# Optimization experiments

Measured on AMD Instinct MI355X. Metric: run time of the kernel, lower is better.

Reference implementation:

```python
import jax, jax.numpy as jnp
import numpy as np

N_NODES = 200000
D = 256
HID = 512
OUT = 2
NUM_GRAPHS = 512


def setup_inputs() -> dict:
    key = jax.random.key(0)
    ks = jax.random.split(key, 8)
    x = jax.random.normal(ks[0], (N_NODES, D), dtype=jnp.float32)
    batch = jnp.sort(jax.random.randint(ks[1], (N_NODES,), 0, NUM_GRAPHS, dtype=jnp.int32))
    # MLP params (Linear stores weight as [out, in] in torch; we use [in, out])
    W1 = jax.random.normal(ks[2], (D, HID), dtype=jnp.float32) / np.sqrt(D)
    b1 = jnp.zeros((HID,), dtype=jnp.float32)
    W2 = jax.random.normal(ks[3], (HID, HID), dtype=jnp.float32) / np.sqrt(HID)
    b2 = jnp.zeros((HID,), dtype=jnp.float32)
    W3 = jax.random.normal(ks[4], (HID, OUT), dtype=jnp.float32) / np.sqrt(HID)
    b3 = jnp.zeros((OUT,), dtype=jnp.float32)
    return {"final_node_embeddings": x, "batch_vector": batch,
            "W1": W1, "b1": b1, "W2": W2, "b2": b2, "W3": W3, "b3": b3}


def reference(final_node_embeddings, batch_vector, W1, b1, W2, b2, W3, b3):
    x = final_node_embeddings
    # segment max pooling over graphs; empty graphs -> zeros (matches original)
    seg = jax.ops.segment_max(x, batch_vector, num_segments=NUM_GRAPHS)  # [G, D]
    counts = jax.ops.segment_sum(jnp.ones((x.shape[0],), dtype=x.dtype),
                                 batch_vector, num_segments=NUM_GRAPHS)  # [G]
    g = jnp.where(counts[:, None] > 0, seg, jnp.zeros((), dtype=x.dtype))
    # readout MLP (dropout inactive at inference)
    h = jax.nn.relu(g @ W1 + b1)
    h = jax.nn.relu(h @ W2 + b2)
    return h @ W3 + b3
```

## Files before the change

### kernel.cpp

```cpp
#include <hip/hip_runtime.h>
#include <float.h>

#define N_NODES 200000
#define D 256
#define HID 512
#define OUTD 2
#define NG 512

__global__ void k_bounds(const int* __restrict__ batch, int* __restrict__ row_start, int n) {
    int i = blockIdx.x * blockDim.x + threadIdx.x;
    if (i >= n) return;
    int b  = batch[i];
    int bp = (i == 0) ? -1 : batch[i - 1];
    for (int g = bp + 1; g <= b; ++g) row_start[g] = i;
    if (i == n - 1) {
        for (int g = b + 1; g <= NG; ++g) row_start[g] = n;
    }
}

__device__ __forceinline__ float4 fmax4(float4 a, float4 b) {
    return make_float4(fmaxf(a.x, b.x), fmaxf(a.y, b.y), fmaxf(a.z, b.z), fmaxf(a.w, b.w));
}

__global__ __launch_bounds__(256) void k_main(const float* __restrict__ x,
                                              const int* __restrict__ rs,
                                              const float* __restrict__ W1,
                                              const float* __restrict__ b1,
                                              const float* __restrict__ W2,
                                              const float* __restrict__ b2,
                                              const float* __restrict__ W3,
                                              const float* __restrict__ b3,
                                              float* __restrict__ out) {
    const int t    = threadIdx.x;
    const int lane = t & 63;
    const int wave = t >> 6;
    const int g0   = blockIdx.x * 2;

    __shared__ float g_row[2][D];
    __shared__ float h1s[2][HID];
    __shared__ float h2s[2][HID];
    __shared__ float4 red[4][64];
    __shared__ float fin[4][4];

    const float* xc = x + (size_t)lane * 4;
#pragma unroll
    for (int gi = 0; gi < 2; ++gi) {
        const int r0 = rs[g0 + gi];
        const int r1 = rs[g0 + gi + 1];
        float4 m = make_float4(-FLT_MAX, -FLT_MAX, -FLT_MAX, -FLT_MAX);
        int r = r0 + wave;
        for (; r + 28 < r1; r += 32) {
            float4 v0 = *reinterpret_cast<const float4*>(xc + (size_t)(r)      * D);
            float4 v1 = *reinterpret_cast<const float4*>(xc + (size_t)(r + 4)  * D);
            float4 v2 = *reinterpret_cast<const float4*>(xc + (size_t)(r + 8)  * D);
            float4 v3 = *reinterpret_cast<const float4*>(xc + (size_t)(r + 12) * D);
            float4 v4 = *reinterpret_cast<const float4*>(xc + (size_t)(r + 16) * D);
            float4 v5 = *reinterpret_cast<const float4*>(xc + (size_t)(r + 20) * D);
            float4 v6 = *reinterpret_cast<const float4*>(xc + (size_t)(r + 24) * D);
            float4 v7 = *reinterpret_cast<const float4*>(xc + (size_t)(r + 28) * D);
            m = fmax4(m, fmax4(fmax4(fmax4(v0, v1), fmax4(v2, v3)),
                               fmax4(fmax4(v4, v5), fmax4(v6, v7))));
        }
        for (; r < r1; r += 4) {
            float4 v = *reinterpret_cast<const float4*>(xc + (size_t)r * D);
            m = fmax4(m, v);
        }
        __syncthreads();
        red[wave][lane] = m;
        __syncthreads();
        if (wave == 0) {
            float4 o = fmax4(fmax4(red[0][lane], red[1][lane]),
                             fmax4(red[2][lane], red[3][lane]));
            if (r1 == r0) o = make_float4(0.f, 0.f, 0.f, 0.f);
            *reinterpret_cast<float4*>(&g_row[gi][lane * 4]) = o;
        }
    }
    __syncthreads();

    {
        float a00 = 0.f, a01 = 0.f, a10 = 0.f, a11 = 0.f;
        const float* w = W1 + 2 * t;
#pragma unroll 8
        for (int k = 0; k < D; k += 4) {
            float4 ga = *reinterpret_cast<const float4*>(&g_row[0][k]);
            float4 gb = *reinterpret_cast<const float4*>(&g_row[1][k]);
            float2 w0 = *reinterpret_cast<const float2*>(w + (size_t)(k)     * HID);
            float2 w1 = *reinterpret_cast<const float2*>(w + (size_t)(k + 1) * HID);
            float2 w2 = *reinterpret_cast<const float2*>(w + (size_t)(k + 2) * HID);
            float2 w3 = *reinterpret_cast<const float2*>(w + (size_t)(k + 3) * HID);
            a00 += ga.x * w0.x; a01 += ga.x * w0.y; a10 += gb.x * w0.x; a11 += gb.x * w0.y;
            a00 += ga.y * w1.x; a01 += ga.y * w1.y; a10 += gb.y * w1.x; a11 += gb.y * w1.y;
            a00 += ga.z * w2.x; a01 += ga.z * w2.y; a10 += gb.z * w2.x; a11 += gb.z * w2.y;
            a00 += ga.w * w3.x; a01 += ga.w * w3.y; a10 += gb.w * w3.x; a11 += gb.w * w3.y;
        }
        float2 bb = *reinterpret_cast<const float2*>(b1 + 2 * t);
        *reinterpret_cast<float2*>(&h1s[0][2 * t]) =
            make_float2(fmaxf(a00 + bb.x, 0.f), fmaxf(a01 + bb.y, 0.f));
        *reinterpret_cast<float2*>(&h1s[1][2 * t]) =
            make_float2(fmaxf(a10 + bb.x, 0.f), fmaxf(a11 + bb.y, 0.f));
    }
    __syncthreads();

    {
        float a00 = 0.f, a01 = 0.f, a10 = 0.f, a11 = 0.f;
        const float* w = W2 + 2 * t;
#pragma unroll 8
        for (int k = 0; k < HID; k += 4) {
            float4 ga = *reinterpret_cast<const float4*>(&h1s[0][k]);
            float4 gb = *reinterpret_cast<const float4*>(&h1s[1][k]);
            float2 w0 = *reinterpret_cast<const float2*>(w + (size_t)(k)     * HID);
            float2 w1 = *reinterpret_cast<const float2*>(w + (size_t)(k + 1) * HID);
            float2 w2 = *reinterpret_cast<const float2*>(w + (size_t)(k + 2) * HID);
            float2 w3 = *reinterpret_cast<const float2*>(w + (size_t)(k + 3) * HID);
            a00 += ga.x * w0.x; a01 += ga.x * w0.y; a10 += gb.x * w0.x; a11 += gb.x * w0.y;
            a00 += ga.y * w1.x; a01 += ga.y * w1.y; a10 += gb.y * w1.x; a11 += gb.y * w1.y;
            a00 += ga.z * w2.x; a01 += ga.z * w2.y; a10 += gb.z * w2.x; a11 += gb.z * w2.y;
            a00 += ga.w * w3.x; a01 += ga.w * w3.y; a10 += gb.w * w3.x; a11 += gb.w * w3.y;
        }
        float2 bb = *reinterpret_cast<const float2*>(b2 + 2 * t);
        *reinterpret_cast<float2*>(&h2s[0][2 * t]) =
            make_float2(fmaxf(a00 + bb.x, 0.f), fmaxf(a01 + bb.y, 0.f));
        *reinterpret_cast<float2*>(&h2s[1][2 * t]) =
            make_float2(fmaxf(a10 + bb.x, 0.f), fmaxf(a11 + bb.y, 0.f));
    }
    __syncthreads();

    {
        float4 w = *reinterpret_cast<const float4*>(W3 + 4 * t);
        float2 ha = *reinterpret_cast<const float2*>(&h2s[0][2 * t]);
        float2 hb = *reinterpret_cast<const float2*>(&h2s[1][2 * t]);
        float p00 = ha.x * w.x + ha.y * w.z;
        float p01 = ha.x * w.y + ha.y * w.w;
        float p10 = hb.x * w.x + hb.y * w.z;
        float p11 = hb.x * w.y + hb.y * w.w;
#pragma unroll
        for (int off = 32; off; off >>= 1) {
            p00 += __shfl_xor(p00, off);
            p01 += __shfl_xor(p01, off);
            p10 += __shfl_xor(p10, off);
            p11 += __shfl_xor(p11, off);
        }
        if (lane == 0) {
            fin[wave][0] = p00; fin[wave][1] = p01;
            fin[wave][2] = p10; fin[wave][3] = p11;
        }
        __syncthreads();
        if (t < 4) {
            float s = fin[0][t] + fin[1][t] + fin[2][t] + fin[3][t];
            out[(size_t)(g0 + (t >> 1)) * OUTD + (t & 1)] = s + b3[t & 1];
        }
    }
}

extern "C" void kernel_launch(void* const* d_in, const int* in_sizes, int n_in,
                              void* d_out, int out_size, void* d_ws, size_t ws_size,
                              hipStream_t stream) {
    const float* x     = (const float*)d_in[0];
    const int*   batch = (const int*)d_in[1];
    const float* W1    = (const float*)d_in[2];
    const float* b1    = (const float*)d_in[3];
    const float* W2    = (const float*)d_in[4];
    const float* b2    = (const float*)d_in[5];
    const float* W3    = (const float*)d_in[6];
    const float* b3    = (const float*)d_in[7];
    float* out = (float*)d_out;

    int* row_start = (int*)d_ws;

    k_bounds<<<(N_NODES + 255) / 256, 256, 0, stream>>>(batch, row_start, N_NODES);
    k_main<<<NG / 2, 256, 0, stream>>>(x, row_start, W1, b1, W2, b2, W3, b3, out);
}
```

Before: 66.84 us.

## Split pooling into row-parallel atomic-max pass and separate batched MLP kernel

Replaces the per-graph pooling (256 blocks, each scanning its own two segments) with a row-partitioned pool over 2048 blocks. Each block max-reduces its rows per segment and merges partial maxima into global memory with atomicMax on order-preserving encoded floats. A separate MLP kernel decodes the pooled rows and processes 4 graphs per block, so each W1/W2 read serves more graphs. The goal is to spread the 200MB read across far more blocks; the cost is an extra init launch plus atomic traffic at segment boundaries.

```diff
diff --git a/kernel.cpp b/kernel.cpp
--- a/kernel.cpp
+++ b/kernel.cpp
@@ -6,50 +6,58 @@
 #define HID 512
 #define OUTD 2
 #define NG 512
-
-__global__ void k_bounds(const int* __restrict__ batch, int* __restrict__ row_start, int n) {
-    int i = blockIdx.x * blockDim.x + threadIdx.x;
-    if (i >= n) return;
-    int b  = batch[i];
-    int bp = (i == 0) ? -1 : batch[i - 1];
-    for (int g = bp + 1; g <= b; ++g) row_start[g] = i;
-    if (i == n - 1) {
-        for (int g = b + 1; g <= NG; ++g) row_start[g] = n;
-    }
+#define POOL_BLOCKS 2048
+#define ROWS_PER_BLK ((N_NODES + POOL_BLOCKS - 1) / POOL_BLOCKS)
+
+__device__ __forceinline__ unsigned enc_f32(float f) {
+    unsigned u = __float_as_uint(f);
+    return (u & 0x80000000u) ? ~u : (u | 0x80000000u);
+}
+__device__ __forceinline__ float dec_f32(unsigned u) {
+    if (u == 0u) return 0.f;
+    unsigned b = (u & 0x80000000u) ? (u & 0x7FFFFFFFu) : ~u;
+    return __uint_as_float(b);
 }
 
 __device__ __forceinline__ float4 fmax4(float4 a, float4 b) {
     return make_float4(fmaxf(a.x, b.x), fmaxf(a.y, b.y), fmaxf(a.z, b.z), fmaxf(a.w, b.w));
 }
 
-__global__ __launch_bounds__(256) void k_main(const float* __restrict__ x,
-                                              const int* __restrict__ rs,
-                                              const float* __restrict__ W1,
-                                              const float* __restrict__ b1,
-                                              const float* __restrict__ W2,
-                                              const float* __restrict__ b2,
-                                              const float* __restrict__ W3,
-                                              const float* __restrict__ b3,
-                                              float* __restrict__ out) {
-    const int t    = threadIdx.x;
-    const int lane = t & 63;
-    const int wave = t >> 6;
-    const int g0   = blockIdx.x * 2;
-
-    __shared__ float g_row[2][D];
-    __shared__ float h1s[2][HID];
-    __shared__ float h2s[2][HID];
-    __shared__ float4 red[4][64];
-    __shared__ float fin[4][4];
-
+__global__ void k_init(uint4* __restrict__ gp4) {
+    gp4[blockIdx.x * blockDim.x + threadIdx.x] = make_uint4(0u, 0u, 0u, 0u);
+}
+
+__global__ __launch_bounds__(256) void k_pool(const float* __restrict__ x,
+                                              const int* __restrict__ batch,
+                                              unsigned* __restrict__ gp) {
+    const int lane = threadIdx.x & 63;
+    const int wave = threadIdx.x >> 6;
+    const int rbeg = blockIdx.x * ROWS_PER_BLK;
+    const int rend = min(rbeg + ROWS_PER_BLK, N_NODES);
     const float* xc = x + (size_t)lane * 4;
-#pragma unroll
-    for (int gi = 0; gi < 2; ++gi) {
-        const int r0 = rs[g0 + gi];
-        const int r1 = rs[g0 + gi + 1];
-        float4 m = make_float4(-FLT_MAX, -FLT_MAX, -FLT_MAX, -FLT_MAX);
-        int r = r0 + wave;
-        for (; r + 28 < r1; r += 32) {
+
+    const float4 NEUT = make_float4(-FLT_MAX, -FLT_MAX, -FLT_MAX, -FLT_MAX);
+    float4 m = NEUT;
+    int cur = -1;
+
+    auto flush = [&](int g, float4 mm) {
+        unsigned* p = gp + (size_t)g * D + lane * 4;
+        atomicMax(p + 0, enc_f32(mm.x));
+        atomicMax(p + 1, enc_f32(mm.y));
+        atomicMax(p + 2, enc_f32(mm.z));
+        atomicMax(p + 3, enc_f32(mm.w));
+    };
+
+    int r = rbeg + wave;
+    while (r < rend) {
+        const int rl = r + 28;
+        if (rl < rend && batch[r] == batch[rl]) {
+            const int bg = batch[r];
+            if (bg != cur) {
+                if (cur >= 0) flush(cur, m);
+                m = NEUT;
+                cur = bg;
+            }
             float4 v0 = *reinterpret_cast<const float4*>(xc + (size_t)(r)      * D);
             float4 v1 = *reinterpret_cast<const float4*>(xc + (size_t)(r + 4)  * D);
             float4 v2 = *reinterpret_cast<const float4*>(xc + (size_t)(r + 8)  * D);
@@ -60,94 +68,137 @@
             float4 v7 = *reinterpret_cast<const float4*>(xc + (size_t)(r + 28) * D);
             m = fmax4(m, fmax4(fmax4(fmax4(v0, v1), fmax4(v2, v3)),
                                fmax4(fmax4(v4, v5), fmax4(v6, v7))));
-        }
-        for (; r < r1; r += 4) {
-            float4 v = *reinterpret_cast<const float4*>(xc + (size_t)r * D);
-            m = fmax4(m, v);
-        }
-        __syncthreads();
-        red[wave][lane] = m;
-        __syncthreads();
-        if (wave == 0) {
-            float4 o = fmax4(fmax4(red[0][lane], red[1][lane]),
-                             fmax4(red[2][lane], red[3][lane]));
-            if (r1 == r0) o = make_float4(0.f, 0.f, 0.f, 0.f);
-            *reinterpret_cast<float4*>(&g_row[gi][lane * 4]) = o;
-        }
+        } else {
+            float4 v[8];
+            int bg[8];
+            bool ok[8];
+#pragma unroll
+            for (int j = 0; j < 8; ++j) {
+                int rj = r + 4 * j;
+                ok[j] = rj < rend;
+                int rc = ok[j] ? rj : rend - 1;
+                v[j]  = *reinterpret_cast<const float4*>(xc + (size_t)rc * D);
+                bg[j] = batch[rc];
+            }
+#pragma unroll
+            for (int j = 0; j < 8; ++j) {
+                if (ok[j]) {
+                    if (bg[j] != cur) {
+                        if (cur >= 0) flush(cur, m);
+                        m = NEUT;
+                        cur = bg[j];
+                    }
+                    m = fmax4(m, v[j]);
+                }
+            }
+        }
+        r += 32;
+    }
+    if (cur >= 0) flush(cur, m);
+}
+
+__global__ __launch_bounds__(256) void k_mlp(const unsigned* __restrict__ gp,
+                                             const float* __restrict__ W1,
+                                             const float* __restrict__ b1,
+                                             const float* __restrict__ W2,
+                                             const float* __restrict__ b2,
+                                             const float* __restrict__ W3,
+                                             const float* __restrict__ b3,
+                                             float* __restrict__ out) {
+    const int t    = threadIdx.x;
+    const int lane = t & 63;
+    const int wave = t >> 6;
+    const int g0   = blockIdx.x * 4;
+
+    __shared__ float gr[4 * D];
+    __shared__ float h1s[4 * HID];
+    __shared__ float h2s[4 * HID];
+    __shared__ float fin[4][8];
+
+    {
+        uint4 u = reinterpret_cast<const uint4*>(gp + (size_t)g0 * D)[t];
+        float4 f = make_float4(dec_f32(u.x), dec_f32(u.y), dec_f32(u.z), dec_f32(u.w));
+        *reinterpret_cast<float4*>(&gr[t * 4]) = f;
     }
     __syncthreads();
 
     {
-        float a00 = 0.f, a01 = 0.f, a10 = 0.f, a11 = 0.f;
+        float acc[4][2] = {};
         const float* w = W1 + 2 * t;
-#pragma unroll 8
         for (int k = 0; k < D; k += 4) {
-            float4 ga = *reinterpret_cast<const float4*>(&g_row[0][k]);
-            float4 gb = *reinterpret_cast<const float4*>(&g_row[1][k]);
             float2 w0 = *reinterpret_cast<const float2*>(w + (size_t)(k)     * HID);
             float2 w1 = *reinterpret_cast<const float2*>(w + (size_t)(k + 1) * HID);
             float2 w2 = *reinterpret_cast<const float2*>(w + (size_t)(k + 2) * HID);
             float2 w3 = *reinterpret_cast<const float2*>(w + (size_t)(k + 3) * HID);
-            a00 += ga.x * w0.x; a01 += ga.x * w0.y; a10 += gb.x * w0.x; a11 += gb.x * w0.y;
-            a00 += ga.y * w1.x; a01 += ga.y * w1.y; a10 += gb.y * w1.x; a11 += gb.y * w1.y;
-            a00 += ga.z * w2.x; a01 += ga.z * w2.y; a10 += gb.z * w2.x; a11 += gb.z * w2.y;
-            a00 += ga.w * w3.x; a01 += ga.w * w3.y; a10 += gb.w * w3.x; a11 += gb.w * w3.y;
+#pragma unroll
+            for (int p = 0; p < 4; ++p) {
+                float4 a = *reinterpret_cast<const float4*>(&gr[p * D + k]);
+                acc[p][0] += a.x * w0.x + a.y * w1.x + a.z * w2.x + a.w * w3.x;
+                acc[p][1] += a.x * w0.y + a.y * w1.y + a.z * w2.y + a.w * w3.y;
+            }
         }
         float2 bb = *reinterpret_cast<const float2*>(b1 + 2 * t);
-        *reinterpret_cast<float2*>(&h1s[0][2 * t]) =
-            make_float2(fmaxf(a00 + bb.x, 0.f), fmaxf(a01 + bb.y, 0.f));
-        *reinterpret_cast<float2*>(&h1s[1][2 * t]) =
-            make_float2(fmaxf(a10 + bb.x, 0.f), fmaxf(a11 + bb.y, 0.f));
+#pragma unroll
+        for (int p = 0; p < 4; ++p) {
+            h1s[p * HID + 2 * t]     = fmaxf(acc[p][0] + bb.x, 0.f);
+            h1s[p * HID + 2 * t + 1] = fmaxf(acc[p][1] + bb.y, 0.f);
+        }
     }
     __syncthreads();
 
     {
-        float a00 = 0.f, a01 = 0.f, a10 = 0.f, a11 = 0.f;
+        float acc[4][2] = {};
         const float* w = W2 + 2 * t;
-#pragma unroll 8
         for (int k = 0; k < HID; k += 4) {
-            float4 ga = *reinterpret_cast<const float4*>(&h1s[0][k]);
-            float4 gb = *reinterpret_cast<const float4*>(&h1s[1][k]);
             float2 w0 = *reinterpret_cast<const float2*>(w + (size_t)(k)     * HID);
             float2 w1 = *reinterpret_cast<const float2*>(w + (size_t)(k + 1) * HID);
             float2 w2 = *reinterpret_cast<const float2*>(w + (size_t)(k + 2) * HID);
             float2 w3 = *reinterpret_cast<const float2*>(w + (size_t)(k + 3) * HID);
-            a00 += ga.x * w0.x; a01 += ga.x * w0.y; a10 += gb.x * w0.x; a11 += gb.x * w0.y;
-            a00 += ga.y * w1.x; a01 += ga.y * w1.y; a10 += gb.y * w1.x; a11 += gb.y * w1.y;
-            a00 += ga.z * w2.x; a01 += ga.z * w2.y; a10 += gb.z * w2.x; a11 += gb.z * w2.y;
-            a00 += ga.w * w3.x; a01 += ga.w * w3.y; a10 += gb.w * w3.x; a11 += gb.w * w3.y;
+#pragma unroll
+            for (int p = 0; p < 4; ++p) {
+                float4 a = *reinterpret_cast<const float4*>(&h1s[p * HID + k]);
+                acc[p][0] += a.x * w0.x + a.y * w1.x + a.z * w2.x + a.w * w3.x;
+                acc[p][1] += a.x * w0.y + a.y * w1.y + a.z * w2.y + a.w * w3.y;
+            }
         }
         float2 bb = *reinterpret_cast<const float2*>(b2 + 2 * t);
-        *reinterpret_cast<float2*>(&h2s[0][2 * t]) =
-            make_float2(fmaxf(a00 + bb.x, 0.f), fmaxf(a01 + bb.y, 0.f));
-        *reinterpret_cast<float2*>(&h2s[1][2 * t]) =
-            make_float2(fmaxf(a10 + bb.x, 0.f), fmaxf(a11 + bb.y, 0.f));
+#pragma unroll
+        for (int p = 0; p < 4; ++p) {
+            h2s[p * HID + 2 * t]     = fmaxf(acc[p][0] + bb.x, 0.f);
+            h2s[p * HID + 2 * t + 1] = fmaxf(acc[p][1] + bb.y, 0.f);
+        }
     }
     __syncthreads();
 
     {
         float4 w = *reinterpret_cast<const float4*>(W3 + 4 * t);
-        float2 ha = *reinterpret_cast<const float2*>(&h2s[0][2 * t]);
-        float2 hb = *reinterpret_cast<const float2*>(&h2s[1][2 * t]);
-        float p00 = ha.x * w.x + ha.y * w.z;
-        float p01 = ha.x * w.y + ha.y * w.w;
-        float p10 = hb.x * w.x + hb.y * w.z;
-        float p11 = hb.x * w.y + hb.y * w.w;
+        float pv[4][2];
+#pragma unroll
+        for (int p = 0; p < 4; ++p) {
+            float2 h = *reinterpret_cast<const float2*>(&h2s[p * HID + 2 * t]);
+            pv[p][0] = h.x * w.x + h.y * w.z;
+            pv[p][1] = h.x * w.y + h.y * w.w;
+        }
 #pragma unroll
         for (int off = 32; off; off >>= 1) {
-            p00 += __shfl_xor(p00, off);
-            p01 += __shfl_xor(p01, off);
-            p10 += __shfl_xor(p10, off);
-            p11 += __shfl_xor(p11, off);
+#pragma unroll
+            for (int p = 0; p < 4; ++p) {
+                pv[p][0] += __shfl_xor(pv[p][0], off);
+                pv[p][1] += __shfl_xor(pv[p][1], off);
+            }
         }
         if (lane == 0) {
-            fin[wave][0] = p00; fin[wave][1] = p01;
-            fin[wave][2] = p10; fin[wave][3] = p11;
+#pragma unroll
+            for (int p = 0; p < 4; ++p) {
+                fin[wave][p * 2]     = pv[p][0];
+                fin[wave][p * 2 + 1] = pv[p][1];
+            }
         }
         __syncthreads();
-        if (t < 4) {
-            float s = fin[0][t] + fin[1][t] + fin[2][t] + fin[3][t];
-            out[(size_t)(g0 + (t >> 1)) * OUTD + (t & 1)] = s + b3[t & 1];
+        if (t < 8) {
+            int p = t >> 1, c = t & 1;
+            float s = fin[0][t] + fin[1][t] + fin[2][t] + fin[3][t] + b3[c];
+            out[(size_t)(g0 + p) * OUTD + c] = s;
         }
     }
 }
@@ -165,8 +216,9 @@
     const float* b3    = (const float*)d_in[7];
     float* out = (float*)d_out;
 
-    int* row_start = (int*)d_ws;
-
-    k_bounds<<<(N_NODES + 255) / 256, 256, 0, stream>>>(batch, row_start, N_NODES);
-    k_main<<<NG / 2, 256, 0, stream>>>(x, row_start, W1, b1, W2, b2, W3, b3, out);
-}
+    unsigned* gp_enc = (unsigned*)d_ws;
+
+    k_init<<<NG * D / 4 / 256, 256, 0, stream>>>((uint4*)gp_enc);
+    k_pool<<<POOL_BLOCKS, 256, 0, stream>>>(x, batch, gp_enc);
+    k_mlp<<<NG / 4, 256, 0, stream>>>(gp_enc, W1, b1, W2, b2, W3, b3, out);
+}
```

After: 100.7 us. 50.7% more time.
